# Kernel tuning notes

Hardware: AMD Instinct MI355X
Metric: run time of the kernel (lower is better)

Reference implementation:

```python
import jax, jax.numpy as jnp
import numpy as np

N = 50000
E = 800000
D_IN = 128
H = 128
K = 64
BN_EPS = 1e-5


def setup_inputs() -> dict:
    key = jax.random.key(0)
    ks = jax.random.split(key, 16)
    s_in = 1.0 / np.sqrt(D_IN)
    s_h = 1.0 / np.sqrt(H)
    inp = {
        "x": jax.random.normal(ks[0], (N, D_IN), dtype=jnp.float32),
        "edge_index": jax.random.randint(ks[1], (2, E), 0, N, dtype=jnp.int64),
        # GIN layer 1 MLP (Linear(D_IN,H) -> ReLU -> Linear(H,H)), eps1, BN1
        "W1a": jax.random.uniform(ks[2], (D_IN, H), jnp.float32, -s_in, s_in),
        "b1a": jnp.zeros((H,), jnp.float32),
        "W1b": jax.random.uniform(ks[3], (H, H), jnp.float32, -s_h, s_h),
        "b1b": jnp.zeros((H,), jnp.float32),
        "eps1": jnp.zeros((), jnp.float32),
        "gamma1": jnp.ones((H,), jnp.float32),
        "beta1": jnp.zeros((H,), jnp.float32),
        # GIN layer 2 MLP, eps2, BN2
        "W2a": jax.random.uniform(ks[4], (H, H), jnp.float32, -s_h, s_h),
        "b2a": jnp.zeros((H,), jnp.float32),
        "W2b": jax.random.uniform(ks[5], (H, H), jnp.float32, -s_h, s_h),
        "b2b": jnp.zeros((H,), jnp.float32),
        "eps2": jnp.zeros((), jnp.float32),
        "gamma2": jnp.ones((H,), jnp.float32),
        "beta2": jnp.zeros((H,), jnp.float32),
        # final projection (no bias) and learnable log temperature
        "Wout": jax.random.uniform(ks[6], (H, K), jnp.float32, -s_h, s_h),
        "log_tau": jnp.zeros((), jnp.float32),  # log(1.0)
    }
    return inp


def _gin_layer(x, src, dst, Wa, ba, Wb, bb, eps):
    # GINConv: mlp((1+eps)*x + sum_{j in N(i)} x_j), scatter-add over edges
    agg = jax.ops.segment_sum(x[src], dst, num_segments=N)  # [N, d]
    h = (1.0 + eps) * x + agg
    h = jax.nn.relu(h @ Wa + ba) @ Wb + bb
    return h


def _batchnorm(x, gamma, beta):
    # training-mode BatchNorm1d over node dim (biased variance)
    m = jnp.mean(x, axis=0)
    v = jnp.mean(jnp.square(x - m), axis=0)
    return (x - m) * jax.lax.rsqrt(v + BN_EPS) * gamma + beta


def reference(x, edge_index, W1a, b1a, W1b, b1b, eps1, gamma1, beta1,
              W2a, b2a, W2b, b2b, eps2, gamma2, beta2, Wout, log_tau):
    src, dst = edge_index[0], edge_index[1]
    h = _gin_layer(x, src, dst, W1a, b1a, W1b, b1b, eps1)
    h = jax.nn.relu(_batchnorm(h, gamma1, beta1))
    h = _gin_layer(h, src, dst, W2a, b2a, W2b, b2b, eps2)
    h = jax.nn.relu(_batchnorm(h, gamma2, beta2))
    logits = h @ Wout  # [N, K]
    tau = jnp.exp(log_tau)
    S = jax.nn.softmax(logits / tau, axis=-1)
    return (S, logits)
```

## Files before the change

### kernel.cpp

```cpp
#include <hip/hip_runtime.h>
#include <hip/hip_fp16.h>


#define NNODES 50000
#define NEDGES 800000
#define HD 128
#define KOUT 64
#define NCLS 8
#define CLSW 6250
#define HIST_BLKS 512
#define EF_CHUNK 3200

typedef __attribute__((ext_vector_type(8))) _Float16 f16x8;
typedef __attribute__((ext_vector_type(4))) float f32x4;

__device__ __forceinline__ unsigned short f2h_bits(float f) {
    _Float16 h = (_Float16)f;
    return __builtin_bit_cast(unsigned short, h);
}
__device__ __forceinline__ f16x8 h8_relu(f16x8 v) {
    #pragma unroll
    for (int i = 0; i < 8; ++i) v[i] = (v[i] > (_Float16)0.f) ? v[i] : (_Float16)0.f;
    return v;
}

__global__ __launch_bounds__(256) void prep_all(
    const float* __restrict__ x, unsigned short* __restrict__ xh,
    const float* __restrict__ W1a, const float* __restrict__ W1b,
    const float* __restrict__ W2a, const float* __restrict__ W2b,
    unsigned short* __restrict__ wt1a, unsigned short* __restrict__ wt1b,
    unsigned short* __restrict__ wt2a, unsigned short* __restrict__ wt2b,
    const int* __restrict__ ei, int* __restrict__ deg)
{
    __shared__ int h[CLSW];
    int bid = blockIdx.x;
    if (bid < HIST_BLKS) {
        const int cls = bid & 7;
        const int lo = cls * CLSW;
        const int e0 = (bid >> 3) * 12500;
        for (int i = threadIdx.x; i < CLSW; i += 256) h[i] = 0;
        __syncthreads();
        const int4* d4p = (const int4*)(ei + NEDGES) + (e0 >> 2);
        for (int i = threadIdx.x; i < 3125; i += 256) {
            int4 d = d4p[i];
            unsigned a0 = (unsigned)(d.x - lo), a1 = (unsigned)(d.y - lo);
            unsigned a2 = (unsigned)(d.z - lo), a3 = (unsigned)(d.w - lo);
            if (a0 < (unsigned)CLSW) atomicAdd(&h[a0], 1);
            if (a1 < (unsigned)CLSW) atomicAdd(&h[a1], 1);
            if (a2 < (unsigned)CLSW) atomicAdd(&h[a2], 1);
            if (a3 < (unsigned)CLSW) atomicAdd(&h[a3], 1);
        }
        __syncthreads();
        for (int i = threadIdx.x; i < CLSW; i += 256) {
            int v = h[i];
            if (v) atomicAdd(&deg[lo + i], v);
        }
    } else if (bid < HIST_BLKS + 6250) {
        int i = (bid - HIST_BLKS) * 256 + threadIdx.x;
        float4 v = ((const float4*)x)[i];
        ushort4 o;
        o.x = f2h_bits(v.x); o.y = f2h_bits(v.y);
        o.z = f2h_bits(v.z); o.w = f2h_bits(v.w);
        ((ushort4*)xh)[i] = o;
    } else {
        int wb = bid - (HIST_BLKS + 6250);
        int w = wb >> 6;
        int idx = (wb & 63) * 256 + threadIdx.x;
        int n = idx >> 7, k = idx & 127;
        const float* W = (w == 0) ? W1a : (w == 1) ? W1b : (w == 2) ? W2a : W2b;
        unsigned short* Wt = (w == 0) ? wt1a : (w == 1) ? wt1b : (w == 2) ? wt2a : wt2b;
        Wt[idx] = f2h_bits(W[k * HD + n]);
    }
}

__global__ __launch_bounds__(256) void scan_a(
    const int* __restrict__ deg, int* __restrict__ incl, int* __restrict__ bsum)
{
    __shared__ int s[256];
    int t = threadIdx.x, idx = blockIdx.x * 256 + t;
    int v = (idx < NNODES) ? deg[idx] : 0;
    s[t] = v; __syncthreads();
    #pragma unroll
    for (int off = 1; off < 256; off <<= 1) {
        int tmp = (t >= off) ? s[t - off] : 0;
        __syncthreads();
        s[t] += tmp;
        __syncthreads();
    }
    if (idx < NNODES) incl[idx] = s[t];
    if (t == 255) bsum[blockIdx.x] = s[255];
}

__global__ __launch_bounds__(256) void scan_c(
    const int* __restrict__ deg, const int* __restrict__ incl,
    const int* __restrict__ bsum,
    int* __restrict__ row_start, int* __restrict__ cur)
{
    __shared__ int s[256];
    int b = blockIdx.x, t = threadIdx.x;
    int p = 0;
    for (int i = t; i < b; i += 256) p += bsum[i];
    s[t] = p; __syncthreads();
    #pragma unroll
    for (int off = 128; off > 0; off >>= 1) {
        if (t < off) s[t] += s[t + off];
        __syncthreads();
    }
    int off0 = s[0];
    int idx = b * 256 + t;
    if (idx >= NNODES) return;
    int ex = incl[idx] - deg[idx] + off0;
    row_start[idx] = ex;
    cur[idx] = ex;
}

__global__ __launch_bounds__(256) void edge_fill(
    const int* __restrict__ ei, int* __restrict__ cur, int* __restrict__ col)
{
    const int cls = blockIdx.x & 7;
    const int e0 = (blockIdx.x >> 3) * EF_CHUNK;
    const int4* d4p = (const int4*)(ei + NEDGES) + (e0 >> 2);
    const int4* s4p = (const int4*)ei + (e0 >> 2);
    for (int i = threadIdx.x; i < EF_CHUNK / 4; i += 256) {
        int4 d = d4p[i];
        int4 s = s4p[i];
        if (d.x / CLSW == cls) { int p = atomicAdd(&cur[d.x], 1); col[p] = s.x; }
        if (d.y / CLSW == cls) { int p = atomicAdd(&cur[d.y], 1); col[p] = s.y; }
        if (d.z / CLSW == cls) { int p = atomicAdd(&cur[d.z], 1); col[p] = s.z; }
        if (d.w / CLSW == cls) { int p = atomicAdd(&cur[d.w], 1); col[p] = s.w; }
    }
}

template<bool BN>
__global__ __launch_bounds__(256) void gin_gather_w(
    const unsigned short* __restrict__ Xh, const int* __restrict__ col,
    const int* __restrict__ rs, const int* __restrict__ re,
    const float* __restrict__ eps,
    const float* __restrict__ scale, const float* __restrict__ shift,
    unsigned short* __restrict__ H0h)
{
    const int t = threadIdx.x;
    const int g = t >> 4;
    const int lane = t & 15;
    const f16x8* X8 = (const f16x8*)Xh;
    const float alphaf = 1.f + eps[0];

    f16x8 sc8, sh8, al8;
    #pragma unroll
    for (int i = 0; i < 8; ++i) al8[i] = (_Float16)alphaf;
    if (BN) {
        #pragma unroll
        for (int i = 0; i < 8; ++i) {
            sc8[i] = (_Float16)scale[lane * 8 + i];
            sh8[i] = (_Float16)shift[lane * 8 + i];
        }
    }

    #pragma unroll 1
    for (int nn = 0; nn < 2; ++nn) {
        int node = blockIdx.x * 32 + nn * 16 + g;
        if (node >= NNODES) continue;

        f16x8 acc = X8[(long)node * 16 + lane];
        if (BN) acc = h8_relu(acc * sc8 + sh8);
        acc = acc * al8;

        int j = rs[node], end = re[node];
        for (; j + 7 < end; j += 8) {
            int c0 = col[j],     c1 = col[j + 1], c2 = col[j + 2], c3 = col[j + 3];
            int c4 = col[j + 4], c5 = col[j + 5], c6 = col[j + 6], c7 = col[j + 7];
            f16x8 u0 = X8[(long)c0 * 16 + lane];
            f16x8 u1 = X8[(long)c1 * 16 + lane];
            f16x8 u2 = X8[(long)c2 * 16 + lane];
            f16x8 u3 = X8[(long)c3 * 16 + lane];
            f16x8 u4 = X8[(long)c4 * 16 + lane];
            f16x8 u5 = X8[(long)c5 * 16 + lane];
            f16x8 u6 = X8[(long)c6 * 16 + lane];
            f16x8 u7 = X8[(long)c7 * 16 + lane];
            if (BN) {
                u0 = h8_relu(u0 * sc8 + sh8); u1 = h8_relu(u1 * sc8 + sh8);
                u2 = h8_relu(u2 * sc8 + sh8); u3 = h8_relu(u3 * sc8 + sh8);
                u4 = h8_relu(u4 * sc8 + sh8); u5 = h8_relu(u5 * sc8 + sh8);
                u6 = h8_relu(u6 * sc8 + sh8); u7 = h8_relu(u7 * sc8 + sh8);
            }
            acc += ((u0 + u1) + (u2 + u3)) + ((u4 + u5) + (u6 + u7));
        }
        for (; j + 3 < end; j += 4) {
            f16x8 u0 = X8[(long)col[j]     * 16 + lane];
            f16x8 u1 = X8[(long)col[j + 1] * 16 + lane];
            f16x8 u2 = X8[(long)col[j + 2] * 16 + lane];
            f16x8 u3 = X8[(long)col[j + 3] * 16 + lane];
            if (BN) {
                u0 = h8_relu(u0 * sc8 + sh8); u1 = h8_relu(u1 * sc8 + sh8);
                u2 = h8_relu(u2 * sc8 + sh8); u3 = h8_relu(u3 * sc8 + sh8);
            }
            acc += (u0 + u1) + (u2 + u3);
        }
        for (; j < end; ++j) {
            f16x8 u = X8[(long)col[j] * 16 + lane];
            if (BN) u = h8_relu(u * sc8 + sh8);
            acc += u;
        }

        ((f16x8*)H0h)[(long)node * 16 + lane] = acc;
    }
}

__global__ __launch_bounds__(512) void mlp_mfma(
    const unsigned short* __restrict__ A,
    const unsigned short* __restrict__ Wta,
    const float* __restrict__ biasa,
    const unsigned short* __restrict__ Wtb,
    const float* __restrict__ biasb,
    unsigned short* __restrict__ Cb,
    float* __restrict__ Cf,
    float* __restrict__ out_sum, float* __restrict__ out_sq)
{
    __shared__ float4 smem4[69632 / 16];
    char* smem = (char*)smem4;
    _Float16 (*Wsa)[136]  = (_Float16(*)[136])smem;
    _Float16 (*Wsb)[136]  = (_Float16(*)[136])(smem + 34816);
    _Float16 (*Cs16)[136] = (_Float16(*)[136])smem;
    float (*CsF)[132]     = (float(*)[132])smem;
    float* redp           = (float*)smem;

    const int t = threadIdx.x;
    const int wave = t >> 6, lane = t & 63;
    const int m16 = lane & 15, quad = lane >> 4;
    const int row0 = blockIdx.x * 128;
    const int arow = row0 + wave * 16 + m16;

    #pragma unroll
    for (int i = 0; i < 4; ++i) {
        int idx = t + i * 512;
        int r = idx >> 4, s = idx & 15;
        *(float4*)&Wsa[r][s * 8] = ((const float4*)Wta)[idx];
        *(float4*)&Wsb[r][s * 8] = ((const float4*)Wtb)[idx];
    }

    f16x8 afrag[4];
    if (arow < NNODES) {
        const _Float16* ar = (const _Float16*)A + (long)arow * HD + quad * 8;
        #pragma unroll
        for (int kc = 0; kc < 4; ++kc)
            afrag[kc] = *(const f16x8*)(ar + kc * 32);
    } else {
        #pragma unroll
        for (int kc = 0; kc < 4; ++kc)
            afrag[kc] = f16x8{0, 0, 0, 0, 0, 0, 0, 0};
    }
    __syncthreads();

    f32x4 accs[8];
    #pragma unroll
    for (int np = 0; np < 8; np += 2) {
        f32x4 a0 = {0.f, 0.f, 0.f, 0.f};
        f32x4 a1 = {0.f, 0.f, 0.f, 0.f};
        const _Float16* b0 = &Wsa[np * 16 + m16][quad * 8];
        const _Float16* b1 = &Wsa[(np + 1) * 16 + m16][quad * 8];
        #pragma unroll
        for (int kc = 0; kc < 4; ++kc) {
            f16x8 f0 = *(const f16x8*)(b0 + kc * 32);
            f16x8 f1 = *(const f16x8*)(b1 + kc * 32);
            a0 = __builtin_amdgcn_mfma_f32_16x16x32_f16(afrag[kc], f0, a0, 0, 0, 0);
            a1 = __builtin_amdgcn_mfma_f32_16x16x32_f16(afrag[kc], f1, a1, 0, 0, 0);
        }
        accs[np] = a0; accs[np + 1] = a1;
    }
    __syncthreads();

    #pragma unroll
    for (int np = 0; np < 8; ++np) {
        int c = np * 16 + m16;
        float bb = biasa[c];
        #pragma unroll
        for (int r = 0; r < 4; ++r)
            Cs16[wave * 16 + quad * 4 + r][c] =
                (_Float16)fmaxf(accs[np][r] + bb, 0.f);
    }
    __syncthreads();

    f16x8 afrag2[4];
    {
        const int crow = wave * 16 + m16;
        #pragma unroll
        for (int kc = 0; kc < 4; ++kc)
            afrag2[kc] = *(const f16x8*)&Cs16[crow][quad * 8 + kc * 32];
    }
    #pragma unroll
    for (int np = 0; np < 8; np += 2) {
        f32x4 a0 = {0.f, 0.f, 0.f, 0.f};
        f32x4 a1 = {0.f, 0.f, 0.f, 0.f};
        const _Float16* b0 = &Wsb[np * 16 + m16][quad * 8];
        const _Float16* b1 = &Wsb[(np + 1) * 16 + m16][quad * 8];
        #pragma unroll
        for (int kc = 0; kc < 4; ++kc) {
            f16x8 f0 = *(const f16x8*)(b0 + kc * 32);
            f16x8 f1 = *(const f16x8*)(b1 + kc * 32);
            a0 = __builtin_amdgcn_mfma_f32_16x16x32_f16(afrag2[kc], f0, a0, 0, 0, 0);
            a1 = __builtin_amdgcn_mfma_f32_16x16x32_f16(afrag2[kc], f1, a1, 0, 0, 0);
        }
        accs[np] = a0; accs[np + 1] = a1;
    }
    __syncthreads();

    #pragma unroll
    for (int np = 0; np < 8; ++np) {
        int c = np * 16 + m16;
        float bb = biasb[c];
        #pragma unroll
        for (int r = 0; r < 4; ++r)
            CsF[wave * 16 + quad * 4 + r][c] = accs[np][r] + bb;
    }
    __syncthreads();

    const int s4 = t & 31;
    const int rb = t >> 5;
    float lsum[4] = {}, lsq[4] = {};
    #pragma unroll
    for (int i = 0; i < 8; ++i) {
        int r = rb + i * 16;
        int row = row0 + r;
        float4 v = *(const float4*)&CsF[r][s4 * 4];
        if (row < NNODES) {
            if (Cb) {
                ushort4 o;
                o.x = f2h_bits(v.x); o.y = f2h_bits(v.y);
                o.z = f2h_bits(v.z); o.w = f2h_bits(v.w);
                ((ushort4*)Cb)[(long)row * 32 + s4] = o;
            }
            if (Cf) ((float4*)Cf)[(long)row * 32 + s4] = v;
            lsum[0] += v.x; lsum[1] += v.y; lsum[2] += v.z; lsum[3] += v.w;
            lsq[0] = fmaf(v.x, v.x, lsq[0]);
            lsq[1] = fmaf(v.y, v.y, lsq[1]);
            lsq[2] = fmaf(v.z, v.z, lsq[2]);
            lsq[3] = fmaf(v.w, v.w, lsq[3]);
        }
    }
    __syncthreads();

    #pragma unroll
    for (int j = 0; j < 4; ++j) {
        redp[(0 * 16 + rb) * 128 + s4 * 4 + j] = lsum[j];
        redp[(1 * 16 + rb) * 128 + s4 * 4 + j] = lsq[j];
    }
    __syncthreads();
    if (t < 128) {
        float s = 0.f, q = 0.f;
        #pragma unroll
        for (int g = 0; g < 16; ++g) {
            s += redp[g * 128 + t];
            q += redp[(16 + g) * 128 + t];
        }
        const int cls = blockIdx.x & 7;
        atomicAdd(&out_sum[cls * 128 + t], s);
        atomicAdd(&out_sq[cls * 128 + t],  q);
    }
}

__global__ void bn_prep(const float* __restrict__ ssum, const float* __restrict__ ssq,
                        const float* __restrict__ gamma, const float* __restrict__ beta,
                        float* __restrict__ scale, float* __restrict__ shift)
{
    int c = threadIdx.x;
    float s = 0.f, q = 0.f;
    #pragma unroll
    for (int g = 0; g < 8; ++g) {
        s += ssum[g * 128 + c];
        q += ssq[g * 128 + c];
    }
    const float invN = 1.0f / (float)NNODES;
    float m = s * invN;
    float var = fmaf(-m, m, q * invN);
    float rs = rsqrtf(var + 1e-5f);
    float sc = gamma[c] * rs;
    scale[c] = sc;
    shift[c] = beta[c] - m * sc;
}

__global__ __launch_bounds__(256) void out_proj_softmax(
    const float* __restrict__ H, const float* __restrict__ Wout,
    const float* __restrict__ scale, const float* __restrict__ shift,
    const float* __restrict__ log_tau,
    float* __restrict__ outS, float* __restrict__ outL)
{
    __shared__ float As[HD][20];
    const int t = threadIdx.x;
    const long row0 = (long)blockIdx.x * 16;

    #pragma unroll
    for (int i = 0; i < 8; ++i) {
        int idx = t + i * 256;
        int r = idx >> 7, cc = idx & 127;
        float v = H[(row0 + r) * HD + cc];
        As[cc][r] = fmaxf(fmaf(v, scale[cc], shift[cc]), 0.f);
    }
    __syncthreads();

    const int c = t & 63;
    const int g = t >> 6;
    float acc[4] = {};

    float wq[8];
    #pragma unroll
    for (int i = 0; i < 8; ++i) wq[i] = Wout[i * KOUT + c];

    #pragma unroll 1
    for (int kc = 0; kc < HD; kc += 8) {
        float wn[8];
        if (kc + 8 < HD) {
            #pragma unroll
            for (int i = 0; i < 8; ++i) wn[i] = Wout[(kc + 8 + i) * KOUT + c];
        }
        #pragma unroll
        for (int i = 0; i < 8; ++i) {
            float4 a = *(const float4*)&As[kc + i][g * 4];
            acc[0] = fmaf(a.x, wq[i], acc[0]);
            acc[1] = fmaf(a.y, wq[i], acc[1]);
            acc[2] = fmaf(a.z, wq[i], acc[2]);
            acc[3] = fmaf(a.w, wq[i], acc[3]);
        }
        if (kc + 8 < HD) {
            #pragma unroll
            for (int i = 0; i < 8; ++i) wq[i] = wn[i];
        }
    }

    float inv_tau = __expf(-log_tau[0]);
    #pragma unroll
    for (int i = 0; i < 4; ++i) {
        float z = acc[i] * inv_tau;
        float m = z;
        #pragma unroll
        for (int o = 32; o > 0; o >>= 1) m = fmaxf(m, __shfl_xor(m, o));
        float e = __expf(z - m);
        float s = e;
        #pragma unroll
        for (int o = 32; o > 0; o >>= 1) s += __shfl_xor(s, o);
        long oi = (row0 + g * 4 + i) * KOUT + c;
        outS[oi] = e / s;
        outL[oi] = acc[i];
    }
}

extern "C" void kernel_launch(void* const* d_in, const int* in_sizes, int n_in,
                              void* d_out, int out_size, void* d_ws, size_t ws_size,
                              hipStream_t stream)
{
    const float* x      = (const float*)d_in[0];
    const int*   ei     = (const int*)d_in[1];
    const float* W1a    = (const float*)d_in[2];
    const float* b1a    = (const float*)d_in[3];
    const float* W1b    = (const float*)d_in[4];
    const float* b1b    = (const float*)d_in[5];
    const float* eps1   = (const float*)d_in[6];
    const float* gamma1 = (const float*)d_in[7];
    const float* beta1  = (const float*)d_in[8];
    const float* W2a    = (const float*)d_in[9];
    const float* b2a    = (const float*)d_in[10];
    const float* W2b    = (const float*)d_in[11];
    const float* b2b    = (const float*)d_in[12];
    const float* eps2   = (const float*)d_in[13];
    const float* gamma2 = (const float*)d_in[14];
    const float* beta2  = (const float*)d_in[15];
    const float* Wout   = (const float*)d_in[16];
    const float* ltau   = (const float*)d_in[17];

    const size_t NB = (size_t)NNODES * HD;
    float* B0 = (float*)d_ws;
    float* B1 = B0 + NB;
    float* B2 = B1 + NB;
    float* ST = B2 + NB;
    float* sum1 = ST, *sq1 = ST + 1024, *sum2 = ST + 2048, *sq2 = ST + 3072;
    float* scale1 = ST + 4096, *shift1 = ST + 4224;
    float* scale2 = ST + 4352, *shift2 = ST + 4480;

    unsigned short* xh  = (unsigned short*)B2;
    unsigned short* h0h = (unsigned short*)B0;
    unsigned short* hh  = (unsigned short*)B0;
    unsigned short* h2h = (unsigned short*)B2;

    int* I0        = (int*)(ST + 4608);
    int* deg       = I0;
    int* incl      = I0 + 50048;
    int* row_start = I0 + 2 * 50048;
    int* cur       = I0 + 3 * 50048;
    int* bsum      = I0 + 4 * 50048;
    int* col       = bsum + 256;
    unsigned short* wt1a = (unsigned short*)(col + NEDGES);
    unsigned short* wt1b = wt1a + HD * HD;
    unsigned short* wt2a = wt1b + HD * HD;
    unsigned short* wt2b = wt2a + HD * HD;

    const int SCAN_BLKS = (NNODES + 255) / 256;
    const int GEMM_BLKS = (NNODES + 127) / 128;
    const int GATH_BLKS = (NNODES + 31) / 32;
    const int EF_BLKS   = (NEDGES / EF_CHUNK) * 8;

    hipMemsetAsync(ST, 0, 4096 * sizeof(float), stream);
    hipMemsetAsync(deg, 0, NNODES * sizeof(int), stream);
    prep_all<<<HIST_BLKS + 6506, 256, 0, stream>>>(x, xh, W1a, W1b, W2a, W2b,
                                                   wt1a, wt1b, wt2a, wt2b, ei, deg);
    scan_a<<<SCAN_BLKS, 256, 0, stream>>>(deg, incl, bsum);
    scan_c<<<SCAN_BLKS, 256, 0, stream>>>(deg, incl, bsum, row_start, cur);
    edge_fill<<<EF_BLKS, 256, 0, stream>>>(ei, cur, col);

    gin_gather_w<false><<<GATH_BLKS, 256, 0, stream>>>(
        xh, col, row_start, cur, eps1, nullptr, nullptr, h0h);
    mlp_mfma<<<GEMM_BLKS, 512, 0, stream>>>(
        h0h, wt1a, b1a, wt1b, b1b, hh, nullptr, sum1, sq1);
    bn_prep<<<1, 128, 0, stream>>>(sum1, sq1, gamma1, beta1, scale1, shift1);

    gin_gather_w<true><<<GATH_BLKS, 256, 0, stream>>>(
        hh, col, row_start, cur, eps2, scale1, shift1, h2h);
    mlp_mfma<<<GEMM_BLKS, 512, 0, stream>>>(
        h2h, wt2a, b2a, wt2b, b2b, nullptr, B1, sum2, sq2);
    bn_prep<<<1, 128, 0, stream>>>(sum2, sq2, gamma2, beta2, scale2, shift2);

    out_proj_softmax<<<NNODES / 16, 256, 0, stream>>>(
        B1, Wout, scale2, shift2, ltau,
        (float*)d_out, (float*)d_out + (size_t)NNODES * KOUT);
}
```

Measured before the change: 288.7 us.

## Build CSR with per-chunk histogram offsets instead of global atomic cursors

The histogram blocks now write per-chunk per-node counts instead of atomically adding into a global degree array. A new column-scan kernel turns these into per-chunk exclusive offsets and total degrees. Edge fill then uses LDS atomics plus the precomputed offsets to place each edge, with no global atomics on a cursor array. This removes global atomic contention and the degree memset, at the cost of an extra kernel and a 64×50048 count buffer to read and write.

New measurement: 272.0 us. -5.8%, faster.

```diff
diff --git a/kernel.cpp b/kernel.cpp
--- a/kernel.cpp
+++ b/kernel.cpp
@@ -9,7 +9,9 @@
 #define NCLS 8
 #define CLSW 6250
 #define HIST_BLKS 512
-#define EF_CHUNK 3200
+#define NCHUNK 64
+#define CH_E 12500
+#define NODE_PAD 50048
 
 typedef __attribute__((ext_vector_type(8))) _Float16 f16x8;
 typedef __attribute__((ext_vector_type(4))) float f32x4;
@@ -30,18 +32,19 @@
     const float* __restrict__ W2a, const float* __restrict__ W2b,
     unsigned short* __restrict__ wt1a, unsigned short* __restrict__ wt1b,
     unsigned short* __restrict__ wt2a, unsigned short* __restrict__ wt2b,
-    const int* __restrict__ ei, int* __restrict__ deg)
+    const int* __restrict__ ei, int* __restrict__ cnt)
 {
     __shared__ int h[CLSW];
     int bid = blockIdx.x;
     if (bid < HIST_BLKS) {
         const int cls = bid & 7;
+        const int chunk = bid >> 3;
         const int lo = cls * CLSW;
-        const int e0 = (bid >> 3) * 12500;
+        const int e0 = chunk * CH_E;
         for (int i = threadIdx.x; i < CLSW; i += 256) h[i] = 0;
         __syncthreads();
         const int4* d4p = (const int4*)(ei + NEDGES) + (e0 >> 2);
-        for (int i = threadIdx.x; i < 3125; i += 256) {
+        for (int i = threadIdx.x; i < CH_E / 4; i += 256) {
             int4 d = d4p[i];
             unsigned a0 = (unsigned)(d.x - lo), a1 = (unsigned)(d.y - lo);
             unsigned a2 = (unsigned)(d.z - lo), a3 = (unsigned)(d.w - lo);
@@ -51,10 +54,9 @@
             if (a3 < (unsigned)CLSW) atomicAdd(&h[a3], 1);
         }
         __syncthreads();
-        for (int i = threadIdx.x; i < CLSW; i += 256) {
-            int v = h[i];
-            if (v) atomicAdd(&deg[lo + i], v);
-        }
+        int* crow = cnt + chunk * NODE_PAD + lo;
+        for (int i = threadIdx.x; i < CLSW; i += 256)
+            crow[i] = h[i];
     } else if (bid < HIST_BLKS + 6250) {
         int i = (bid - HIST_BLKS) * 256 + threadIdx.x;
         float4 v = ((const float4*)x)[i];
@@ -73,6 +75,22 @@
     }
 }
 
+__global__ __launch_bounds__(256) void cscan(
+    int* __restrict__ cnt, int* __restrict__ deg)
+{
+    int node = blockIdx.x * 256 + threadIdx.x;
+    if (node >= NNODES) return;
+    int* p = cnt + node;
+    int run = 0;
+    #pragma unroll 8
+    for (int c = 0; c < NCHUNK; ++c) {
+        int v = p[(long)c * NODE_PAD];
+        p[(long)c * NODE_PAD] = run;
+        run += v;
+    }
+    deg[node] = run;
+}
+
 __global__ __launch_bounds__(256) void scan_a(
     const int* __restrict__ deg, int* __restrict__ incl, int* __restrict__ bsum)
 {
@@ -94,7 +112,7 @@
 __global__ __launch_bounds__(256) void scan_c(
     const int* __restrict__ deg, const int* __restrict__ incl,
     const int* __restrict__ bsum,
-    int* __restrict__ row_start, int* __restrict__ cur)
+    int* __restrict__ row_start, int* __restrict__ row_end)
 {
     __shared__ int s[256];
     int b = blockIdx.x, t = threadIdx.x;
@@ -109,25 +127,46 @@
     int off0 = s[0];
     int idx = b * 256 + t;
     if (idx >= NNODES) return;
-    int ex = incl[idx] - deg[idx] + off0;
-    row_start[idx] = ex;
-    cur[idx] = ex;
+    int inc = incl[idx];
+    row_start[idx] = inc - deg[idx] + off0;
+    row_end[idx] = inc + off0;
 }
 
 __global__ __launch_bounds__(256) void edge_fill(
-    const int* __restrict__ ei, int* __restrict__ cur, int* __restrict__ col)
-{
+    const int* __restrict__ ei, const int* __restrict__ rs,
+    const int* __restrict__ cnt, int* __restrict__ col)
+{
+    __shared__ int h[CLSW];
     const int cls = blockIdx.x & 7;
-    const int e0 = (blockIdx.x >> 3) * EF_CHUNK;
+    const int chunk = blockIdx.x >> 3;
+    const int lo = cls * CLSW;
+    const int e0 = chunk * CH_E;
+    const int* cb = cnt + chunk * NODE_PAD;
+    for (int i = threadIdx.x; i < CLSW; i += 256) h[i] = 0;
+    __syncthreads();
     const int4* d4p = (const int4*)(ei + NEDGES) + (e0 >> 2);
     const int4* s4p = (const int4*)ei + (e0 >> 2);
-    for (int i = threadIdx.x; i < EF_CHUNK / 4; i += 256) {
+    for (int i = threadIdx.x; i < CH_E / 4; i += 256) {
         int4 d = d4p[i];
         int4 s = s4p[i];
-        if (d.x / CLSW == cls) { int p = atomicAdd(&cur[d.x], 1); col[p] = s.x; }
-        if (d.y / CLSW == cls) { int p = atomicAdd(&cur[d.y], 1); col[p] = s.y; }
-        if (d.z / CLSW == cls) { int p = atomicAdd(&cur[d.z], 1); col[p] = s.z; }
-        if (d.w / CLSW == cls) { int p = atomicAdd(&cur[d.w], 1); col[p] = s.w; }
+        unsigned a0 = (unsigned)(d.x - lo), a1 = (unsigned)(d.y - lo);
+        unsigned a2 = (unsigned)(d.z - lo), a3 = (unsigned)(d.w - lo);
+        if (a0 < (unsigned)CLSW) {
+            int r = atomicAdd(&h[a0], 1);
+            col[rs[d.x] + cb[d.x] + r] = s.x;
+        }
+        if (a1 < (unsigned)CLSW) {
+            int r = atomicAdd(&h[a1], 1);
+            col[rs[d.y] + cb[d.y] + r] = s.y;
+        }
+        if (a2 < (unsigned)CLSW) {
+            int r = atomicAdd(&h[a2], 1);
+            col[rs[d.z] + cb[d.z] + r] = s.z;
+        }
+        if (a3 < (unsigned)CLSW) {
+            int r = atomicAdd(&h[a3], 1);
+            col[rs[d.w] + cb[d.w] + r] = s.w;
+        }
     }
 }
 
@@ -482,12 +521,13 @@
 
     int* I0        = (int*)(ST + 4608);
     int* deg       = I0;
-    int* incl      = I0 + 50048;
-    int* row_start = I0 + 2 * 50048;
-    int* cur       = I0 + 3 * 50048;
-    int* bsum      = I0 + 4 * 50048;
+    int* incl      = I0 + NODE_PAD;
+    int* row_start = I0 + 2 * NODE_PAD;
+    int* row_end   = I0 + 3 * NODE_PAD;
+    int* bsum      = I0 + 4 * NODE_PAD;
     int* col       = bsum + 256;
-    unsigned short* wt1a = (unsigned short*)(col + NEDGES);
+    int* cnt       = col + NEDGES;
+    unsigned short* wt1a = (unsigned short*)(cnt + NCHUNK * NODE_PAD);
     unsigned short* wt1b = wt1a + HD * HD;
     unsigned short* wt2a = wt1b + HD * HD;
     unsigned short* wt2b = wt2a + HD * HD;
@@ -495,24 +535,23 @@
     const int SCAN_BLKS = (NNODES + 255) / 256;
     const int GEMM_BLKS = (NNODES + 127) / 128;
     const int GATH_BLKS = (NNODES + 31) / 32;
-    const int EF_BLKS   = (NEDGES / EF_CHUNK) * 8;
 
     hipMemsetAsync(ST, 0, 4096 * sizeof(float), stream);
-    hipMemsetAsync(deg, 0, NNODES * sizeof(int), stream);
     prep_all<<<HIST_BLKS + 6506, 256, 0, stream>>>(x, xh, W1a, W1b, W2a, W2b,
-                                                   wt1a, wt1b, wt2a, wt2b, ei, deg);
+                                                   wt1a, wt1b, wt2a, wt2b, ei, cnt);
+    cscan<<<SCAN_BLKS, 256, 0, stream>>>(cnt, deg);
     scan_a<<<SCAN_BLKS, 256, 0, stream>>>(deg, incl, bsum);
-    scan_c<<<SCAN_BLKS, 256, 0, stream>>>(deg, incl, bsum, row_start, cur);
-    edge_fill<<<EF_BLKS, 256, 0, stream>>>(ei, cur, col);
+    scan_c<<<SCAN_BLKS, 256, 0, stream>>>(deg, incl, bsum, row_start, row_end);
+    edge_fill<<<HIST_BLKS, 256, 0, stream>>>(ei, row_start, cnt, col);
 
     gin_gather_w<false><<<GATH_BLKS, 256, 0, stream>>>(
-        xh, col, row_start, cur, eps1, nullptr, nullptr, h0h);
+        xh, col, row_start, row_end, eps1, nullptr, nullptr, h0h);
     mlp_mfma<<<GEMM_BLKS, 512, 0, stream>>>(
         h0h, wt1a, b1a, wt1b, b1b, hh, nullptr, sum1, sq1);
     bn_prep<<<1, 128, 0, stream>>>(sum1, sq1, gamma1, beta1, scale1, shift1);
 
     gin_gather_w<true><<<GATH_BLKS, 256, 0, stream>>>(
-        hh, col, row_start, cur, eps2, scale1, shift1, h2h);
+        hh, col, row_start, row_end, eps2, scale1, shift1, h2h);
     mlp_mfma<<<GEMM_BLKS, 512, 0, stream>>>(
         h2h, wt2a, b2a, wt2b, b2b, nullptr, B1, sum2, sq2);
     bn_prep<<<1, 128, 0, stream>>>(sum2, sq2, gamma2, beta2, scale2, shift2);
```
